# Kernel optimization log

Hardware: AMD Instinct MI355X
Metric: run time of the kernel (lower is better)

Reference implementation:

```python
import jax, jax.numpy as jnp
import numpy as np

B, IN, OUT, NUM_F = 131072, 128, 128, 8


def setup_inputs() -> dict:
    key = jax.random.key(0)
    ks = jax.random.split(key, 6)
    x = jax.random.normal(ks[0], (B, IN), dtype=jnp.float32)
    grid = jnp.arange(NUM_F, dtype=jnp.float32) + 1.0            # nn.Parameter(arange(num_f)+1)
    base_weight = jax.random.normal(ks[1], (OUT, IN), dtype=jnp.float32) * 0.05
    scale_sp = jnp.ones((OUT,), dtype=jnp.float32)
    coef = jax.random.uniform(ks[2], (IN, NUM_F), dtype=jnp.float32)  # torch.rand
    # Conv1d(in=IN*NUM_F, out=OUT*NUM_F, k=1, groups=NUM_F) == per-frequency [OUT, IN] matmul
    fan_in = IN  # per-group in-channels * kernel_size(1)
    bound = 1.0 / np.sqrt(fan_in)
    conv_w = jax.random.uniform(ks[3], (NUM_F, OUT, IN), dtype=jnp.float32,
                                minval=-bound, maxval=bound)
    conv_b = jax.random.uniform(ks[4], (NUM_F, OUT), dtype=jnp.float32,
                                minval=-bound, maxval=bound)
    return {"x": x, "grid": grid, "base_weight": base_weight,
            "scale_sp": scale_sp, "coef": coef, "conv_w": conv_w, "conv_b": conv_b}


def reference(x, grid, base_weight, scale_sp, coef, conv_w, conv_b):
    # base path: SiLU(x) @ W_base^T  -> [B, OUT]
    base_out = jax.nn.silu(x) @ base_weight.T
    # Fourier basis: sin(grid_f * x_i) -> [B, F, I]
    s = jnp.sin(x[:, None, :] * grid[None, :, None])
    # coef [I, F] broadcast-multiplied per (i, f)
    s = s * coef.T[None, :, :]                      # [B, F, I]
    # grouped 1x1 conv == per-frequency matmul, plus per-(f, o) bias
    spline = jnp.einsum('bfi,foi->bfo', s, conv_w) + conv_b[None, :, :]  # [B, F, OUT]
    spline_out = spline.sum(axis=1) * scale_sp      # [B, OUT]
    return base_out + spline_out
```

## Files before the change

### kernel.cpp

```cpp
#include <hip/hip_runtime.h>
#include <stdint.h>

#define NCHUNK 9
#define IN_DIM 128
#define OUT_DIM 128
#define NUM_F 8
#define CHUNK_ELEMS (OUT_DIM * IN_DIM)
#define W_ELEMS (NCHUNK * CHUNK_ELEMS)
#define B_TOTAL 131072

typedef __bf16 bf16x8 __attribute__((ext_vector_type(8)));
typedef float floatx16 __attribute__((ext_vector_type(16)));

__device__ __forceinline__ int widx(int c, int o, int i) {
  int s = i >> 4, q2 = (i >> 3) & 1, j = i & 7;
  return (((c * 8 + s) * 2 + q2) * 128 + o) * 8 + j;
}

__device__ __forceinline__ unsigned short f2bf_rn(float f) {
  unsigned u = __builtin_bit_cast(unsigned, f);
  u += 0x7FFFu + ((u >> 16) & 1u);
  return (unsigned short)(u >> 16);
}

__global__ void skan_prep(const float* __restrict__ base_w,
                          const float* __restrict__ scale_sp,
                          const float* __restrict__ coef,
                          const float* __restrict__ conv_w,
                          const float* __restrict__ conv_b,
                          unsigned short* __restrict__ Wall,
                          float* __restrict__ bias) {
  int b = blockIdx.x;
  int i = threadIdx.x;
  if (b < NCHUNK * OUT_DIM) {
    int c = b >> 7;
    int o = b & 127;
    float v;
    if (c == 0) {
      v = base_w[o * IN_DIM + i];
    } else {
      int f = c - 1;
      v = conv_w[(f * OUT_DIM + o) * IN_DIM + i] * coef[i * NUM_F + f] * scale_sp[o];
    }
    Wall[widx(c, o, i)] = f2bf_rn(v);
  } else {
    float s = 0.f;
#pragma unroll
    for (int f = 0; f < NUM_F; ++f) s += conv_b[f * OUT_DIM + i];
    bias[i] = s * scale_sp[i];
  }
}

__device__ __forceinline__ unsigned pack2(float lo, float hi) {
  unsigned ulo = __builtin_bit_cast(unsigned, lo) + 0x8000u;
  unsigned uhi = __builtin_bit_cast(unsigned, hi) + 0x8000u;
  return __builtin_amdgcn_perm(uhi, ulo, 0x07060302u);
}

__device__ __forceinline__ bf16x8 pack_frag(const float* v) {
  union { unsigned u[4]; bf16x8 f; } r;
  r.u[0] = pack2(v[0], v[1]);
  r.u[1] = pack2(v[2], v[3]);
  r.u[2] = pack2(v[4], v[5]);
  r.u[3] = pack2(v[6], v[7]);
  return r.f;
}

__device__ __forceinline__ float silu(float v) {
  return v * __builtin_amdgcn_rcpf(1.f + __expf(-v));
}

__global__ __launch_bounds__(256, 2)
void skan_main(const float* __restrict__ x,
               const unsigned short* __restrict__ Wall,
               const float* __restrict__ bias,
               float* __restrict__ out) {
  const int tid  = threadIdx.x;
  const int lane = tid & 63;
  const int w    = tid >> 6;
  const int m    = lane & 31;
  const int q2   = lane >> 5;
  const int rowBase = blockIdx.x * 128 + (w & 1) * 64;
  const int colBase = (w >> 1) * 64;

  const int wl_base = q2 * 1024 + (colBase + m) * 8;

  floatx16 acc[2][2];
#pragma unroll
  for (int mt = 0; mt < 2; ++mt)
#pragma unroll
    for (int nt = 0; nt < 2; ++nt)
#pragma unroll
      for (int e = 0; e < 16; ++e) acc[mt][nt][e] = 0.f;

  const float* xr0 = x + (size_t)(rowBase + m) * IN_DIM;
  const float* xr1 = xr0 + 32 * IN_DIM;

#pragma unroll 1
  for (int sg = 0; sg < 4; ++sg) {
    float xv[2][2][8];
#pragma unroll
    for (int mt = 0; mt < 2; ++mt) {
      const float4* p = (const float4*)((mt ? xr1 : xr0) + sg * 32 + q2 * 8);
#pragma unroll
      for (int s2 = 0; s2 < 2; ++s2) {
        float4 a = p[s2 * 4];
        float4 b = p[s2 * 4 + 1];
        xv[mt][s2][0] = a.x; xv[mt][s2][1] = a.y;
        xv[mt][s2][2] = a.z; xv[mt][s2][3] = a.w;
        xv[mt][s2][4] = b.x; xv[mt][s2][5] = b.y;
        xv[mt][s2][6] = b.z; xv[mt][s2][7] = b.w;
      }
    }

    int4 Bb[2][4];
    const int sgrow = sg * 2;
#define LOADB(dst, c)                                                        \
    {                                                                        \
      _Pragma("unroll")                                                      \
      for (int s2 = 0; s2 < 2; ++s2)                                         \
        _Pragma("unroll")                                                    \
        for (int nt = 0; nt < 2; ++nt)                                       \
          dst[s2 * 2 + nt] = *(const int4*)(Wall +                           \
              ((c) * 16 + (sgrow + s2) * 2) * 1024 + nt * 256 + wl_base);    \
    }

    LOADB(Bb[0], 0);

    {
      float sv[2][2][8];
#pragma unroll
      for (int mt = 0; mt < 2; ++mt)
#pragma unroll
        for (int s2 = 0; s2 < 2; ++s2)
#pragma unroll
          for (int j = 0; j < 8; ++j) sv[mt][s2][j] = silu(xv[mt][s2][j]);

      LOADB(Bb[1], 1);
#pragma unroll
      for (int s2 = 0; s2 < 2; ++s2) {
        bf16x8 a0 = pack_frag(sv[0][s2]);
        bf16x8 a1 = pack_frag(sv[1][s2]);
#pragma unroll
        for (int nt = 0; nt < 2; ++nt) {
          bf16x8 bf = __builtin_bit_cast(bf16x8, Bb[0][s2 * 2 + nt]);
          acc[0][nt] = __builtin_amdgcn_mfma_f32_32x32x16_bf16(a0, bf, acc[0][nt], 0, 0, 0);
          acc[1][nt] = __builtin_amdgcn_mfma_f32_32x32x16_bf16(a1, bf, acc[1][nt], 0, 0, 0);
        }
      }
    }

    float sp[32], spp[32], c2[32];
#pragma unroll
    for (int mt = 0; mt < 2; ++mt)
#pragma unroll
      for (int s2 = 0; s2 < 2; ++s2)
#pragma unroll
        for (int j = 0; j < 8; ++j) {
          int v = (mt * 2 + s2) * 8 + j;
          float xx = xv[mt][s2][j];
          sp[v]  = __sinf(xx);
          c2[v]  = 2.f * __cosf(xx);
          spp[v] = 0.f;
        }

#pragma unroll
    for (int c = 1; c <= 8; ++c) {
      const int cur = c & 1;
      if (c < 8) LOADB(Bb[cur ^ 1], c + 1);

      if (c >= 2) {
#pragma unroll
        for (int v = 0; v < 32; ++v) {
          float t = __builtin_fmaf(c2[v], sp[v], -spp[v]);
          spp[v] = sp[v];
          sp[v] = t;
        }
      }
#pragma unroll
      for (int s2 = 0; s2 < 2; ++s2) {
        bf16x8 a0 = pack_frag(&sp[(0 * 2 + s2) * 8]);
        bf16x8 a1 = pack_frag(&sp[(1 * 2 + s2) * 8]);
#pragma unroll
        for (int nt = 0; nt < 2; ++nt) {
          bf16x8 bf = __builtin_bit_cast(bf16x8, Bb[cur][s2 * 2 + nt]);
          acc[0][nt] = __builtin_amdgcn_mfma_f32_32x32x16_bf16(a0, bf, acc[0][nt], 0, 0, 0);
          acc[1][nt] = __builtin_amdgcn_mfma_f32_32x32x16_bf16(a1, bf, acc[1][nt], 0, 0, 0);
        }
      }
    }
#undef LOADB
  }

#pragma unroll
  for (int mt = 0; mt < 2; ++mt) {
    float* obase = out + (size_t)(rowBase + mt * 32) * OUT_DIM + colBase + m;
#pragma unroll
    for (int nt = 0; nt < 2; ++nt) {
      float bv = bias[colBase + nt * 32 + m];
#pragma unroll
      for (int e = 0; e < 16; ++e) {
        int rl = (e & 3) + 8 * (e >> 2) + 4 * q2;
        obase[(size_t)rl * OUT_DIM + nt * 32] = acc[mt][nt][e] + bv;
      }
    }
  }
}

extern "C" void kernel_launch(void* const* d_in, const int* in_sizes, int n_in,
                              void* d_out, int out_size, void* d_ws, size_t ws_size,
                              hipStream_t stream) {
  const float* x      = (const float*)d_in[0];
  const float* base_w = (const float*)d_in[2];
  const float* scale  = (const float*)d_in[3];
  const float* coef   = (const float*)d_in[4];
  const float* conv_w = (const float*)d_in[5];
  const float* conv_b = (const float*)d_in[6];

  unsigned short* Wall = (unsigned short*)d_ws;
  float* bias = (float*)((char*)d_ws + (size_t)W_ELEMS * 2);
  float* out  = (float*)d_out;

  skan_prep<<<NCHUNK * OUT_DIM + 1, 128, 0, stream>>>(base_w, scale, coef,
                                                      conv_w, conv_b, Wall, bias);
  skan_main<<<B_TOTAL / 128, 256, 0, stream>>>(x, Wall, bias, out);
}
```

Baseline: 168.8 us.

## Stage sine-path weights in LDS via async global_load_lds and widen per-wave tiles

Each block now covers 256 rows, and each wave computes a full 64x128 output tile instead of 64x64. The sine-path weights are repacked per input-slice group and copied asynchronously into a 64KB shared buffer with global_load_lds, then read from LDS in the Chebyshev loop. This cuts redundant global/L2 weight traffic across waves and halves the grid. In exchange it adds block-wide barriers, more accumulator registers (8 tiles), and LDS usage that may limit occupancy.

```diff
diff --git a/kernel.cpp b/kernel.cpp
--- a/kernel.cpp
+++ b/kernel.cpp
@@ -5,17 +5,17 @@
 #define IN_DIM 128
 #define OUT_DIM 128
 #define NUM_F 8
-#define CHUNK_ELEMS (OUT_DIM * IN_DIM)
-#define W_ELEMS (NCHUNK * CHUNK_ELEMS)
 #define B_TOTAL 131072
+
+#define WBASE_ELEMS (OUT_DIM * IN_DIM)
+#define WSIN_ELEMS (8 * OUT_DIM * IN_DIM)
+#define SG_SLICE 32768
 
 typedef __bf16 bf16x8 __attribute__((ext_vector_type(8)));
 typedef float floatx16 __attribute__((ext_vector_type(16)));
 
-__device__ __forceinline__ int widx(int c, int o, int i) {
-  int s = i >> 4, q2 = (i >> 3) & 1, j = i & 7;
-  return (((c * 8 + s) * 2 + q2) * 128 + o) * 8 + j;
-}
+typedef __attribute__((address_space(1))) const unsigned int gas_u32;
+typedef __attribute__((address_space(3))) unsigned int las_u32;
 
 __device__ __forceinline__ unsigned short f2bf_rn(float f) {
   unsigned u = __builtin_bit_cast(unsigned, f);
@@ -28,21 +28,25 @@
                           const float* __restrict__ coef,
                           const float* __restrict__ conv_w,
                           const float* __restrict__ conv_b,
-                          unsigned short* __restrict__ Wall,
+                          unsigned short* __restrict__ Wbase,
+                          unsigned short* __restrict__ Wsin,
                           float* __restrict__ bias) {
   int b = blockIdx.x;
   int i = threadIdx.x;
+  int j = i & 7, q2 = (i >> 3) & 1;
   if (b < NCHUNK * OUT_DIM) {
     int c = b >> 7;
     int o = b & 127;
-    float v;
     if (c == 0) {
-      v = base_w[o * IN_DIM + i];
+      float v = base_w[o * IN_DIM + i];
+      int s = i >> 4;
+      Wbase[(s * 2 + q2) * 1024 + o * 8 + j] = f2bf_rn(v);
     } else {
       int f = c - 1;
-      v = conv_w[(f * OUT_DIM + o) * IN_DIM + i] * coef[i * NUM_F + f] * scale_sp[o];
-    }
-    Wall[widx(c, o, i)] = f2bf_rn(v);
+      float v = conv_w[(f * OUT_DIM + o) * IN_DIM + i] * coef[i * NUM_F + f] * scale_sp[o];
+      int sg = i >> 5, s2 = (i >> 4) & 1;
+      Wsin[((sg * 8 + f) * 4 + s2 * 2 + q2) * 1024 + o * 8 + j] = f2bf_rn(v);
+    }
   } else {
     float s = 0.f;
 #pragma unroll
@@ -72,24 +76,26 @@
 
 __global__ __launch_bounds__(256, 2)
 void skan_main(const float* __restrict__ x,
-               const unsigned short* __restrict__ Wall,
+               const unsigned short* __restrict__ Wbase,
+               const unsigned short* __restrict__ Wsin,
                const float* __restrict__ bias,
                float* __restrict__ out) {
+  __shared__ unsigned short sB[SG_SLICE];
+
   const int tid  = threadIdx.x;
   const int lane = tid & 63;
   const int w    = tid >> 6;
   const int m    = lane & 31;
   const int q2   = lane >> 5;
-  const int rowBase = blockIdx.x * 128 + (w & 1) * 64;
-  const int colBase = (w >> 1) * 64;
-
-  const int wl_base = q2 * 1024 + (colBase + m) * 8;
-
-  floatx16 acc[2][2];
+  const int rowBase = blockIdx.x * 256 + w * 64;
+
+  const int fragCol = m * 8;
+
+  floatx16 acc[2][4];
 #pragma unroll
   for (int mt = 0; mt < 2; ++mt)
 #pragma unroll
-    for (int nt = 0; nt < 2; ++nt)
+    for (int nt = 0; nt < 4; ++nt)
 #pragma unroll
       for (int e = 0; e < 16; ++e) acc[mt][nt][e] = 0.f;
 
@@ -98,14 +104,26 @@
 
 #pragma unroll 1
   for (int sg = 0; sg < 4; ++sg) {
+    {
+      const char* src = (const char*)(Wsin + sg * SG_SLICE);
+      char* dst = (char*)sB;
+      int off = tid * 16;
+#pragma unroll
+      for (int it = 0; it < 16; ++it) {
+        __builtin_amdgcn_global_load_lds((gas_u32*)(src + off), (las_u32*)(dst + off),
+                                         16, 0, 0);
+        off += 4096;
+      }
+    }
+
     float xv[2][2][8];
 #pragma unroll
     for (int mt = 0; mt < 2; ++mt) {
-      const float4* p = (const float4*)((mt ? xr1 : xr0) + sg * 32 + q2 * 8);
+      const float* xr = mt ? xr1 : xr0;
 #pragma unroll
       for (int s2 = 0; s2 < 2; ++s2) {
-        float4 a = p[s2 * 4];
-        float4 b = p[s2 * 4 + 1];
+        float4 a = *(const float4*)(xr + sg * 32 + s2 * 16 + q2 * 8);
+        float4 b = *(const float4*)(xr + sg * 32 + s2 * 16 + q2 * 8 + 4);
         xv[mt][s2][0] = a.x; xv[mt][s2][1] = a.y;
         xv[mt][s2][2] = a.z; xv[mt][s2][3] = a.w;
         xv[mt][s2][4] = b.x; xv[mt][s2][5] = b.y;
@@ -113,51 +131,38 @@
       }
     }
 
-    int4 Bb[2][4];
-    const int sgrow = sg * 2;
-#define LOADB(dst, c)                                                        \
-    {                                                                        \
-      _Pragma("unroll")                                                      \
-      for (int s2 = 0; s2 < 2; ++s2)                                         \
-        _Pragma("unroll")                                                    \
-        for (int nt = 0; nt < 2; ++nt)                                       \
-          dst[s2 * 2 + nt] = *(const int4*)(Wall +                           \
-              ((c) * 16 + (sgrow + s2) * 2) * 1024 + nt * 256 + wl_base);    \
-    }
-
-    LOADB(Bb[0], 0);
-
-    {
-      float sv[2][2][8];
+#pragma unroll
+    for (int s2 = 0; s2 < 2; ++s2) {
+      int4 Bb[4];
+#pragma unroll
+      for (int nt = 0; nt < 4; ++nt)
+        Bb[nt] = *(const int4*)(Wbase + ((sg * 2 + s2) * 2 + q2) * 1024 +
+                                nt * 256 + fragCol);
+      float sv[16];
 #pragma unroll
       for (int mt = 0; mt < 2; ++mt)
 #pragma unroll
-        for (int s2 = 0; s2 < 2; ++s2)
-#pragma unroll
-          for (int j = 0; j < 8; ++j) sv[mt][s2][j] = silu(xv[mt][s2][j]);
-
-      LOADB(Bb[1], 1);
-#pragma unroll
-      for (int s2 = 0; s2 < 2; ++s2) {
-        bf16x8 a0 = pack_frag(sv[0][s2]);
-        bf16x8 a1 = pack_frag(sv[1][s2]);
-#pragma unroll
-        for (int nt = 0; nt < 2; ++nt) {
-          bf16x8 bf = __builtin_bit_cast(bf16x8, Bb[0][s2 * 2 + nt]);
-          acc[0][nt] = __builtin_amdgcn_mfma_f32_32x32x16_bf16(a0, bf, acc[0][nt], 0, 0, 0);
-          acc[1][nt] = __builtin_amdgcn_mfma_f32_32x32x16_bf16(a1, bf, acc[1][nt], 0, 0, 0);
-        }
-      }
-    }
-
-    float sp[32], spp[32], c2[32];
-#pragma unroll
-    for (int mt = 0; mt < 2; ++mt)
-#pragma unroll
-      for (int s2 = 0; s2 < 2; ++s2)
+        for (int j = 0; j < 8; ++j) sv[mt * 8 + j] = silu(xv[mt][s2][j]);
+      bf16x8 a0 = pack_frag(&sv[0]);
+      bf16x8 a1 = pack_frag(&sv[8]);
+#pragma unroll
+      for (int nt = 0; nt < 4; ++nt) {
+        bf16x8 bf = __builtin_bit_cast(bf16x8, Bb[nt]);
+        acc[0][nt] = __builtin_amdgcn_mfma_f32_32x32x16_bf16(a0, bf, acc[0][nt], 0, 0, 0);
+        acc[1][nt] = __builtin_amdgcn_mfma_f32_32x32x16_bf16(a1, bf, acc[1][nt], 0, 0, 0);
+      }
+    }
+
+    __syncthreads();
+
+#pragma unroll
+    for (int s2 = 0; s2 < 2; ++s2) {
+      float sp[16], spp[16], c2[16];
+#pragma unroll
+      for (int mt = 0; mt < 2; ++mt)
 #pragma unroll
         for (int j = 0; j < 8; ++j) {
-          int v = (mt * 2 + s2) * 8 + j;
+          int v = mt * 8 + j;
           float xx = xv[mt][s2][j];
           sp[v]  = __sinf(xx);
           c2[v]  = 2.f * __cosf(xx);
@@ -165,39 +170,40 @@
         }
 
 #pragma unroll
-    for (int c = 1; c <= 8; ++c) {
-      const int cur = c & 1;
-      if (c < 8) LOADB(Bb[cur ^ 1], c + 1);
-
-      if (c >= 2) {
-#pragma unroll
-        for (int v = 0; v < 32; ++v) {
-          float t = __builtin_fmaf(c2[v], sp[v], -spp[v]);
-          spp[v] = sp[v];
-          sp[v] = t;
+      for (int c = 1; c <= 8; ++c) {
+        bf16x8 Bf[4];
+        const unsigned short* bp = sB + ((c - 1) * 4 + s2 * 2 + q2) * 1024 + fragCol;
+#pragma unroll
+        for (int nt = 0; nt < 4; ++nt)
+          Bf[nt] = *(const bf16x8*)(bp + nt * 256);
+
+        if (c >= 2) {
+#pragma unroll
+          for (int v = 0; v < 16; ++v) {
+            float t = __builtin_fmaf(c2[v], sp[v], -spp[v]);
+            spp[v] = sp[v];
+            sp[v] = t;
+          }
         }
-      }
-#pragma unroll
-      for (int s2 = 0; s2 < 2; ++s2) {
-        bf16x8 a0 = pack_frag(&sp[(0 * 2 + s2) * 8]);
-        bf16x8 a1 = pack_frag(&sp[(1 * 2 + s2) * 8]);
-#pragma unroll
-        for (int nt = 0; nt < 2; ++nt) {
-          bf16x8 bf = __builtin_bit_cast(bf16x8, Bb[cur][s2 * 2 + nt]);
-          acc[0][nt] = __builtin_amdgcn_mfma_f32_32x32x16_bf16(a0, bf, acc[0][nt], 0, 0, 0);
-          acc[1][nt] = __builtin_amdgcn_mfma_f32_32x32x16_bf16(a1, bf, acc[1][nt], 0, 0, 0);
+        bf16x8 a0 = pack_frag(&sp[0]);
+        bf16x8 a1 = pack_frag(&sp[8]);
+#pragma unroll
+        for (int nt = 0; nt < 4; ++nt) {
+          acc[0][nt] = __builtin_amdgcn_mfma_f32_32x32x16_bf16(a0, Bf[nt], acc[0][nt], 0, 0, 0);
+          acc[1][nt] = __builtin_amdgcn_mfma_f32_32x32x16_bf16(a1, Bf[nt], acc[1][nt], 0, 0, 0);
         }
       }
     }
-#undef LOADB
+
+    __syncthreads();
   }
 
 #pragma unroll
   for (int mt = 0; mt < 2; ++mt) {
-    float* obase = out + (size_t)(rowBase + mt * 32) * OUT_DIM + colBase + m;
-#pragma unroll
-    for (int nt = 0; nt < 2; ++nt) {
-      float bv = bias[colBase + nt * 32 + m];
+    float* obase = out + (size_t)(rowBase + mt * 32) * OUT_DIM + m;
+#pragma unroll
+    for (int nt = 0; nt < 4; ++nt) {
+      float bv = bias[nt * 32 + m];
 #pragma unroll
       for (int e = 0; e < 16; ++e) {
         int rl = (e & 3) + 8 * (e >> 2) + 4 * q2;
@@ -217,11 +223,12 @@
   const float* conv_w = (const float*)d_in[5];
   const float* conv_b = (const float*)d_in[6];
 
-  unsigned short* Wall = (unsigned short*)d_ws;
-  float* bias = (float*)((char*)d_ws + (size_t)W_ELEMS * 2);
+  unsigned short* Wbase = (unsigned short*)d_ws;
+  unsigned short* Wsin  = Wbase + WBASE_ELEMS;
+  float* bias = (float*)(Wsin + WSIN_ELEMS);
   float* out  = (float*)d_out;
 
   skan_prep<<<NCHUNK * OUT_DIM + 1, 128, 0, stream>>>(base_w, scale, coef,
-                                                      conv_w, conv_b, Wall, bias);
-  skan_main<<<B_TOTAL / 128, 256, 0, stream>>>(x, Wall, bias, out);
-}
+                                                      conv_w, conv_b, Wbase, Wsin, bias);
+  skan_main<<<B_TOTAL / 256, 256, 0, stream>>>(x, Wbase, Wsin, bias, out);
+}
```

New measurement: 147.5 us. 12.6% less time.
